# Performance work log

Hardware: AMD Instinct MI355X
Metric: run time of the kernel (lower is better)

The kernel has to match this reference:

```python
import jax, jax.numpy as jnp
import numpy as np

N = 100000      # nodes
E = 1600000     # edges (avg degree 16)
F_IN = 128
HID = 64
OUT = 40
NB = 10000      # batch_nodes
BN_EPS = 1e-5


def setup_inputs() -> dict:
    key = jax.random.key(0)
    ks = jax.random.split(key, 16)
    inp = {}
    inp["features"] = jax.random.normal(ks[0], (N, F_IN), dtype=jnp.float32)
    inp["edge_index"] = jax.random.randint(ks[1], (2, E), 0, N, dtype=jnp.int32)
    inp["batch_nodes"] = jax.random.randint(ks[2], (NB,), 0, N, dtype=jnp.int32)
    # conv1 params (Glorot-ish scale)
    inp["W1"] = jax.random.normal(ks[3], (F_IN, HID), dtype=jnp.float32) * (1.0 / np.sqrt(F_IN))
    inp["b1"] = jnp.zeros((HID,), jnp.float32)
    inp["k2_1"] = jnp.float32(0.5)   # learnable k^2, init 0.5
    # conv2 params
    inp["W2"] = jax.random.normal(ks[4], (HID, OUT), dtype=jnp.float32) * (1.0 / np.sqrt(HID))
    inp["b2"] = jnp.zeros((OUT,), jnp.float32)
    inp["k2_2"] = jnp.float32(0.5)
    # BatchNorm1d(hid) inference params
    inp["g1"] = jax.random.uniform(ks[5], (HID,), jnp.float32, 0.5, 1.5)
    inp["be1"] = jax.random.normal(ks[6], (HID,), jnp.float32) * 0.1
    inp["m1"] = jax.random.normal(ks[7], (HID,), jnp.float32) * 0.1
    inp["v1"] = jax.random.uniform(ks[8], (HID,), jnp.float32, 0.5, 1.5)
    # BatchNorm1d(out) inference params
    inp["g2"] = jax.random.uniform(ks[9], (OUT,), jnp.float32, 0.5, 1.5)
    inp["be2"] = jax.random.normal(ks[10], (OUT,), jnp.float32) * 0.1
    inp["m2"] = jax.random.normal(ks[11], (OUT,), jnp.float32) * 0.1
    inp["v2"] = jax.random.uniform(ks[12], (OUT,), jnp.float32, 0.5, 1.5)
    return inp


def _gcn_propagate(h, src, dst, n):
    # add self loops
    loop = jnp.arange(n, dtype=src.dtype)
    s = jnp.concatenate([src, loop])
    d = jnp.concatenate([dst, loop])
    # symmetric GCN normalization D^-1/2 A_hat D^-1/2
    deg = jnp.zeros((n,), h.dtype).at[d].add(1.0)
    dinv = jax.lax.rsqrt(deg)  # deg >= 1 thanks to self loops
    coef = dinv[s] * dinv[d]   # [E+N]
    msg = coef[:, None] * h[s]                      # gather  [E+N, C]
    agg = jnp.zeros_like(h).at[d].add(msg)          # scatter [N, C]
    return agg


def _helm_conv(x, W, b, k2, src, dst, n):
    h = x @ W                                   # [N, C_out]
    agg = _gcn_propagate(h, src, dst, n)        # A_hat h
    out = agg + k2 * h + b                      # (A_hat + k^2 I) h + b
    # Helmholtz residual: (A_hat - I + k^2 I) h ~ (-L + k^2) h
    resid = agg - h + k2 * h
    helm_loss = jnp.mean(resid * resid)
    return out, helm_loss


def _bn(x, g, be, m, v):
    return (x - m) * jax.lax.rsqrt(v + BN_EPS) * g + be


def reference(features, edge_index, batch_nodes, W1, b1, k2_1, W2, b2, k2_2,
              g1, be1, m1, v1, g2, be2, m2, v2):
    n = features.shape[0]
    src, dst = edge_index[0], edge_index[1]
    x, helm_loss1 = _helm_conv(features, W1, b1, k2_1, src, dst, n)
    x = jnp.tanh(_bn(x, g1, be1, m1, v1))
    # dropout is identity in eval mode
    x, _ = _helm_conv(x, W2, b2, k2_2, src, dst, n)
    x = jnp.tanh(_bn(x, g2, be2, m2, v2))
    logp = jax.nn.log_softmax(x[batch_nodes], axis=1)
    return (logp, helm_loss1)
```

## Files before the change

kernel.cpp:

```cpp
#include <hip/hip_runtime.h>
#include <math.h>


#define BN_EPS 1e-5f
#define NB_BKT 512
#define RCAP 4608
#define PSTRIDE 6656

typedef __attribute__((ext_vector_type(8))) short bf16x8;
typedef __attribute__((ext_vector_type(4))) float f32x4;

__device__ inline unsigned short f2b(float f) {
    unsigned u = __float_as_uint(f);
    unsigned r = (u + 0x7fffu + ((u >> 16) & 1u)) >> 16;
    return (unsigned short)r;
}
__device__ inline float b2f_lo(unsigned u) { return __uint_as_float(u << 16); }
__device__ inline float b2f_hi(unsigned u) { return __uint_as_float(u & 0xffff0000u); }
__device__ inline unsigned pk2(float a, float b) {
    return (unsigned)f2b(a) | ((unsigned)f2b(b) << 16);
}
__device__ inline float tanh_fast(float x) {
    float e = __expf(2.0f * x);
    return 1.0f - 2.0f * __builtin_amdgcn_rcpf(e + 1.0f);
}

__global__ __launch_bounds__(512) void k_init(unsigned* __restrict__ bcnt,
                                              const float* __restrict__ b1,
                                              const float* __restrict__ g1,
                                              const float* __restrict__ be1,
                                              const float* __restrict__ m1,
                                              const float* __restrict__ v1,
                                              const float* __restrict__ b2,
                                              const float* __restrict__ g2,
                                              const float* __restrict__ be2,
                                              const float* __restrict__ m2,
                                              const float* __restrict__ v2,
                                              float* __restrict__ A1,
                                              float* __restrict__ S1,
                                              float* __restrict__ A2,
                                              float* __restrict__ S2) {
    int t = threadIdx.x;
    bcnt[t] = 0;
    if (t < 64) {
        float a = g1[t] * rsqrtf(v1[t] + BN_EPS);
        A1[t] = a;
        S1[t] = (b1[t] - m1[t]) * a + be1[t];
    } else if (t < 104) {
        int c = t - 64;
        float a = g2[c] * rsqrtf(v2[c] + BN_EPS);
        A2[c] = a;
        S2[c] = (b2[c] - m2[c]) * a + be2[c];
    }
}

__global__ __launch_bounds__(256) void k_part(const int* __restrict__ src,
                                              const int* __restrict__ dst, int e,
                                              unsigned* __restrict__ bcnt,
                                              unsigned* __restrict__ part, int nblk) {
    __shared__ unsigned h[NB_BKT];
    __shared__ unsigned gbase[NB_BKT];
    __shared__ unsigned cur[NB_BKT];
    int chunk = ((e + nblk - 1) / nblk + 3) & ~3;
    int c0 = blockIdx.x * chunk;
    int c1 = min(c0 + chunk, e);
    if (c0 >= e) return;
    for (int i = threadIdx.x; i < NB_BKT; i += 256) h[i] = 0;
    __syncthreads();
    for (int i = c0 + threadIdx.x * 4; i < c1; i += 1024) {
        if (i + 3 < c1) {
            int4 d = *(const int4*)&dst[i];
            atomicAdd(&h[(unsigned)d.x >> 8], 1u);
            atomicAdd(&h[(unsigned)d.y >> 8], 1u);
            atomicAdd(&h[(unsigned)d.z >> 8], 1u);
            atomicAdd(&h[(unsigned)d.w >> 8], 1u);
        } else {
            for (int j = i; j < c1; ++j) atomicAdd(&h[(unsigned)dst[j] >> 8], 1u);
        }
    }
    __syncthreads();
    for (int i = threadIdx.x; i < NB_BKT; i += 256) {
        unsigned c = h[i];
        gbase[i] = c ? (i * RCAP + atomicAdd(&bcnt[i], c)) : 0u;
        cur[i] = 0;
    }
    __syncthreads();
    for (int i = c0 + threadIdx.x * 4; i < c1; i += 1024) {
        if (i + 3 < c1) {
            int4 s = *(const int4*)&src[i];
            int4 d = *(const int4*)&dst[i];
            unsigned b0 = (unsigned)d.x >> 8, b1 = (unsigned)d.y >> 8;
            unsigned b2 = (unsigned)d.z >> 8, b3 = (unsigned)d.w >> 8;
            unsigned p0 = gbase[b0] + atomicAdd(&cur[b0], 1u);
            unsigned p1 = gbase[b1] + atomicAdd(&cur[b1], 1u);
            unsigned p2 = gbase[b2] + atomicAdd(&cur[b2], 1u);
            unsigned p3 = gbase[b3] + atomicAdd(&cur[b3], 1u);
            if (p0 < (b0 + 1) * RCAP) part[p0] = (((unsigned)d.x & 255u) << 24) | (unsigned)s.x;
            if (p1 < (b1 + 1) * RCAP) part[p1] = (((unsigned)d.y & 255u) << 24) | (unsigned)s.y;
            if (p2 < (b2 + 1) * RCAP) part[p2] = (((unsigned)d.z & 255u) << 24) | (unsigned)s.z;
            if (p3 < (b3 + 1) * RCAP) part[p3] = (((unsigned)d.w & 255u) << 24) | (unsigned)s.w;
        } else {
            for (int j = i; j < c1; ++j) {
                unsigned b = (unsigned)dst[j] >> 8;
                unsigned p = gbase[b] + atomicAdd(&cur[b], 1u);
                if (p < (b + 1) * RCAP)
                    part[p] = (((unsigned)dst[j] & 255u) << 24) | (unsigned)src[j];
            }
        }
    }
}

__global__ __launch_bounds__(256) void k_deg(const unsigned* __restrict__ part,
                                             const unsigned* __restrict__ bcnt,
                                             unsigned long long* __restrict__ rowinfo,
                                             float* __restrict__ dinv, int n) {
    __shared__ unsigned hist[256];
    __shared__ unsigned sc[256];
    int b = blockIdx.x;
    int cnt = (int)min(bcnt[b], (unsigned)RCAP);
    unsigned base = b * RCAP;
    int dst0 = b << 8;
    int nloc = min(256, n - dst0);
    int t = threadIdx.x;
    hist[t] = 0;
    __syncthreads();
    for (int i = t; i < cnt; i += 256) atomicAdd(&hist[part[base + i] >> 24], 1u);
    __syncthreads();
    unsigned c = hist[t];
    unsigned pcnt = (t < nloc) ? ((c + 7u) & ~7u) : 0u;
    sc[t] = pcnt;
    __syncthreads();
    for (int off = 1; off < 256; off <<= 1) {
        unsigned a = (t >= off) ? sc[t - off] : 0u;
        __syncthreads();
        sc[t] += a;
        __syncthreads();
    }
    if (t < nloc) {
        unsigned beg = (unsigned)b * PSTRIDE + (sc[t] - pcnt);
        rowinfo[dst0 + t] = (unsigned long long)beg | ((unsigned long long)pcnt << 32);
        dinv[dst0 + t] = rsqrtf((float)(c + 1u));
    }
}

__global__ __launch_bounds__(256) void k_scatter(const unsigned* __restrict__ part,
                                                 const unsigned* __restrict__ bcnt,
                                                 const unsigned long long* __restrict__ rowinfo,
                                                 const float* __restrict__ dinv,
                                                 uint2* __restrict__ pairs, int n) {
    __shared__ unsigned cur[256];
    __shared__ unsigned pend[256];
    int b = blockIdx.x;
    int cnt = (int)min(bcnt[b], (unsigned)RCAP);
    unsigned base = b * RCAP;
    int dst0 = b << 8;
    int nloc = min(256, n - dst0);
    int t = threadIdx.x;
    if (t < nloc) {
        unsigned long long ri = rowinfo[dst0 + t];
        cur[t] = (unsigned)ri;
        pend[t] = (unsigned)ri + (unsigned)(ri >> 32);
    } else {
        cur[t] = 0;
        pend[t] = 0;
    }
    __syncthreads();
    for (int i = t; i < cnt; i += 256) {
        unsigned p = part[base + i];
        unsigned loc = p >> 24;
        unsigned s = p & 0xFFFFFFu;
        unsigned pos = atomicAdd(&cur[loc], 1u);
        pairs[pos] = make_uint2(s, __float_as_uint(dinv[s]));
    }
    __syncthreads();
    if (t < nloc) {
        for (unsigned pos = cur[t]; pos < pend[t]; ++pos) pairs[pos] = make_uint2(0u, 0u);
    }
}

__global__ __launch_bounds__(256) void k_gemm1(const float* __restrict__ X,
                                               const float* __restrict__ W,
                                               unsigned* __restrict__ H, int n) {
    __shared__ short wb[4][4][64][8];
    __shared__ float cbuf[4][16][65];
    int t = threadIdx.x;
    for (int s = t; s < 1024; s += 256) {
        int l = s & 63, nt = (s >> 6) & 3, kt = s >> 8;
        int kbase = kt * 32 + ((l >> 4) << 3);
        int nn = nt * 16 + (l & 15);
        bf16x8 v;
#pragma unroll
        for (int j = 0; j < 8; ++j) v[j] = (short)f2b(W[(kbase + j) * 64 + nn]);
        *(bf16x8*)&wb[kt][nt][l][0] = v;
    }
    __syncthreads();
    int lane = t & 63, wave = t >> 6;
    int quad = lane >> 4, m = lane & 15;
    int r0 = blockIdx.x * 64 + wave * 16;
    f32x4 acc[4];
#pragma unroll
    for (int i = 0; i < 4; ++i) acc[i] = (f32x4){0.f, 0.f, 0.f, 0.f};
    int rr = min(r0 + m, n - 1);
    const float* xrow = X + (size_t)rr * 128;
#pragma unroll
    for (int kt = 0; kt < 4; ++kt) {
        int kb = kt * 32 + quad * 8;
        float4 x0 = *(const float4*)&xrow[kb];
        float4 x1 = *(const float4*)&xrow[kb + 4];
        bf16x8 af;
        af[0] = (short)f2b(x0.x); af[1] = (short)f2b(x0.y);
        af[2] = (short)f2b(x0.z); af[3] = (short)f2b(x0.w);
        af[4] = (short)f2b(x1.x); af[5] = (short)f2b(x1.y);
        af[6] = (short)f2b(x1.z); af[7] = (short)f2b(x1.w);
#pragma unroll
        for (int nt = 0; nt < 4; ++nt) {
            bf16x8 bf = *(bf16x8*)&wb[kt][nt][lane][0];
            acc[nt] = __builtin_amdgcn_mfma_f32_16x16x32_bf16(af, bf, acc[nt], 0, 0, 0);
        }
    }
#pragma unroll
    for (int nt = 0; nt < 4; ++nt)
#pragma unroll
        for (int r = 0; r < 4; ++r)
            cbuf[wave][quad * 4 + r][nt * 16 + m] = acc[nt][r];
    __syncthreads();
#pragma unroll
    for (int i = 0; i < 8; ++i) {
        int f = i * 64 + lane;
        int row = f >> 5, cp = f & 31;
        int grow = r0 + row;
        if (grow < n)
            H[(size_t)grow * 32 + cp] =
                pk2(cbuf[wave][row][2 * cp], cbuf[wave][row][2 * cp + 1]);
    }
}

__global__ __launch_bounds__(256) void k_gemm2(const unsigned short* __restrict__ X,
                                               const float* __restrict__ W,
                                               unsigned* __restrict__ H, int n) {
    __shared__ short wb[2][3][64][8];
    __shared__ float cbuf[4][16][49];
    int t = threadIdx.x;
    for (int s = t; s < 384; s += 256) {
        int l = s & 63, nt = (s >> 6) % 3, kt = s / 192;
        int kbase = kt * 32 + ((l >> 4) << 3);
        int c = nt * 16 + (l & 15);
        bf16x8 v;
#pragma unroll
        for (int j = 0; j < 8; ++j)
            v[j] = (c < 40) ? (short)f2b(W[(kbase + j) * 40 + c]) : (short)0;
        *(bf16x8*)&wb[kt][nt][l][0] = v;
    }
    __syncthreads();
    int lane = t & 63, wave = t >> 6;
    int quad = lane >> 4, m = lane & 15;
    int r0 = blockIdx.x * 64 + wave * 16;
    f32x4 acc[3];
#pragma unroll
    for (int i = 0; i < 3; ++i) acc[i] = (f32x4){0.f, 0.f, 0.f, 0.f};
    int rr = min(r0 + m, n - 1);
    const unsigned short* xrow = X + (size_t)rr * 64;
#pragma unroll
    for (int kt = 0; kt < 2; ++kt) {
        bf16x8 af = *(const bf16x8*)&xrow[kt * 32 + quad * 8];
#pragma unroll
        for (int nt = 0; nt < 3; ++nt) {
            bf16x8 bf = *(bf16x8*)&wb[kt][nt][lane][0];
            acc[nt] = __builtin_amdgcn_mfma_f32_16x16x32_bf16(af, bf, acc[nt], 0, 0, 0);
        }
    }
#pragma unroll
    for (int nt = 0; nt < 3; ++nt)
#pragma unroll
        for (int r = 0; r < 4; ++r)
            cbuf[wave][quad * 4 + r][nt * 16 + m] = acc[nt][r];
    __syncthreads();
#pragma unroll
    for (int i = 0; i < 5; ++i) {
        int f = i * 64 + lane;
        int row = f / 20, cp = f % 20;
        int grow = r0 + row;
        if (grow < n)
            H[(size_t)grow * 20 + cp] =
                pk2(cbuf[wave][row][2 * cp], cbuf[wave][row][2 * cp + 1]);
    }
}

__global__ __launch_bounds__(256) void k_conv1(const unsigned long long* __restrict__ rowinfo,
                                               const uint2* __restrict__ pairs,
                                               const float* __restrict__ dinv,
                                               const unsigned* __restrict__ h1,
                                               unsigned* __restrict__ x,
                                               const float* __restrict__ A1,
                                               const float* __restrict__ S1,
                                               const float* __restrict__ k2p,
                                               float* __restrict__ partial, int n) {
    int lane = threadIdx.x & 63, wave = threadIdx.x >> 6;
    int half = lane >> 5, c2 = lane & 31;
    int node = blockIdx.x * 4 + wave;
    float r2 = 0.0f;
    if (node < n) {
        unsigned long long ri = rowinfo[node];
        unsigned beg = (unsigned)ri, pdeg = (unsigned)(ri >> 32);
        float dd = dinv[node];
        unsigned hp = h1[(unsigned)node * 32u + (unsigned)c2];
        float hx = b2f_lo(hp), hy = b2f_hi(hp);
        float ax = half ? 0.f : dd * hx;
        float ay = half ? 0.f : dd * hy;
        for (unsigned eb = 0; eb < pdeg; eb += 8) {
            unsigned bi = beg + eb + (unsigned)half * 4u;
            uint4 q0 = *(const uint4*)&pairs[bi];
            uint4 q1 = *(const uint4*)&pairs[bi + 2];
            unsigned p0 = h1[(q0.x << 5) + (unsigned)c2];
            unsigned p1 = h1[(q0.z << 5) + (unsigned)c2];
            unsigned p2 = h1[(q1.x << 5) + (unsigned)c2];
            unsigned p3 = h1[(q1.z << 5) + (unsigned)c2];
            float c0 = __uint_as_float(q0.y), c1 = __uint_as_float(q0.w);
            float c2f = __uint_as_float(q1.y), c3 = __uint_as_float(q1.w);
            ax += c0 * b2f_lo(p0); ay += c0 * b2f_hi(p0);
            ax += c1 * b2f_lo(p1); ay += c1 * b2f_hi(p1);
            ax += c2f * b2f_lo(p2); ay += c2f * b2f_hi(p2);
            ax += c3 * b2f_lo(p3); ay += c3 * b2f_hi(p3);
        }
        ax += __shfl_xor(ax, 32, 64);
        ay += __shfl_xor(ay, 32, 64);
        if (half == 0) {
            float a_x = dd * ax, a_y = dd * ay;
            float k2 = k2p[0];
            float rx = a_x + (k2 - 1.0f) * hx;
            float ry = a_y + (k2 - 1.0f) * hy;
            r2 = rx * rx + ry * ry;
            float2 Ap = *(const float2*)&A1[2 * c2];
            float2 Sp = *(const float2*)&S1[2 * c2];
            float xnx = tanh_fast((a_x + k2 * hx) * Ap.x + Sp.x);
            float xny = tanh_fast((a_y + k2 * hy) * Ap.y + Sp.y);
            x[(unsigned)node * 32u + (unsigned)c2] = pk2(xnx, xny);
        }
    }
    for (int off = 32; off; off >>= 1) r2 += __shfl_xor(r2, off, 64);
    __shared__ float red[4];
    if (lane == 0) red[wave] = r2;
    __syncthreads();
    if (threadIdx.x == 0) partial[blockIdx.x] = red[0] + red[1] + red[2] + red[3];
}

__global__ __launch_bounds__(1024) void k_loss(const float* __restrict__ partial,
                                               int nparts, float* __restrict__ out,
                                               size_t idx, float inv_cnt) {
    float s = 0.f;
    for (int i = threadIdx.x; i < nparts; i += 1024) s += partial[i];
    for (int off = 32; off; off >>= 1) s += __shfl_xor(s, off, 64);
    __shared__ float red[16];
    int wv = threadIdx.x >> 6, ln = threadIdx.x & 63;
    if (ln == 0) red[wv] = s;
    __syncthreads();
    if (threadIdx.x == 0) {
        float t = 0.f;
        for (int i = 0; i < 16; ++i) t += red[i];
        out[idx] = t * inv_cnt;
    }
}

__global__ __launch_bounds__(256) void k_conv2(const int* __restrict__ bn,
                                               const unsigned long long* __restrict__ rowinfo,
                                               const uint2* __restrict__ pairs,
                                               const float* __restrict__ dinv,
                                               const unsigned* __restrict__ h2,
                                               const float* __restrict__ A2,
                                               const float* __restrict__ S2,
                                               const float* __restrict__ k2p,
                                               float* __restrict__ out, int nb) {
    int lane = threadIdx.x & 63, wave = threadIdx.x >> 6;
    int wid = blockIdx.x * 4 + wave;
    if (wid >= nb) return;
    int half = lane >> 5, c2 = lane & 31;
    unsigned p = (unsigned)min(c2, 19);
    int node = bn[wid];
    unsigned long long ri = rowinfo[node];
    unsigned beg = (unsigned)ri, pdeg = (unsigned)(ri >> 32);
    float dd = dinv[node];
    unsigned hp = h2[(unsigned)node * 20u + p];
    float hx = b2f_lo(hp), hy = b2f_hi(hp);
    float ax = half ? 0.f : dd * hx;
    float ay = half ? 0.f : dd * hy;
    for (unsigned eb = 0; eb < pdeg; eb += 8) {
        unsigned bi = beg + eb + (unsigned)half * 4u;
        uint4 q0 = *(const uint4*)&pairs[bi];
        uint4 q1 = *(const uint4*)&pairs[bi + 2];
        unsigned p0 = h2[q0.x * 20u + p];
        unsigned p1 = h2[q0.z * 20u + p];
        unsigned p2 = h2[q1.x * 20u + p];
        unsigned p3 = h2[q1.z * 20u + p];
        float c0 = __uint_as_float(q0.y), c1 = __uint_as_float(q0.w);
        float c2f = __uint_as_float(q1.y), c3 = __uint_as_float(q1.w);
        ax += c0 * b2f_lo(p0); ay += c0 * b2f_hi(p0);
        ax += c1 * b2f_lo(p1); ay += c1 * b2f_hi(p1);
        ax += c2f * b2f_lo(p2); ay += c2f * b2f_hi(p2);
        ax += c3 * b2f_lo(p3); ay += c3 * b2f_hi(p3);
    }
    ax += __shfl_xor(ax, 32, 64);
    ay += __shfl_xor(ay, 32, 64);
    float k2 = k2p[0];
    float2 Ap = *(const float2*)&A2[2 * p];
    float2 Sp = *(const float2*)&S2[2 * p];
    float tx = tanh_fast((dd * ax + k2 * hx) * Ap.x + Sp.x);
    float ty = tanh_fast((dd * ay + k2 * hy) * Ap.y + Sp.y);
    bool act = (half == 0) && (c2 < 20);
    float mx = act ? fmaxf(tx, ty) : -INFINITY;
    for (int off = 32; off; off >>= 1) mx = fmaxf(mx, __shfl_xor(mx, off, 64));
    float es = act ? (__expf(tx - mx) + __expf(ty - mx)) : 0.f;
    for (int off = 32; off; off >>= 1) es += __shfl_xor(es, off, 64);
    if (act) {
        float ls = mx + __logf(es);
        float2 o = make_float2(tx - ls, ty - ls);
        *(float2*)&out[(size_t)wid * 40 + 2 * p] = o;
    }
}

extern "C" void kernel_launch(void* const* d_in, const int* in_sizes, int n_in,
                              void* d_out, int out_size, void* d_ws, size_t ws_size,
                              hipStream_t stream) {
    const float* features = (const float*)d_in[0];
    const int* edge_index = (const int*)d_in[1];
    const int* batch_nodes = (const int*)d_in[2];
    const float* W1 = (const float*)d_in[3];
    const float* b1 = (const float*)d_in[4];
    const float* k2_1 = (const float*)d_in[5];
    const float* W2 = (const float*)d_in[6];
    const float* b2 = (const float*)d_in[7];
    const float* k2_2 = (const float*)d_in[8];
    const float* g1 = (const float*)d_in[9];
    const float* be1 = (const float*)d_in[10];
    const float* m1 = (const float*)d_in[11];
    const float* v1 = (const float*)d_in[12];
    const float* g2 = (const float*)d_in[13];
    const float* be2 = (const float*)d_in[14];
    const float* m2 = (const float*)d_in[15];
    const float* v2 = (const float*)d_in[16];

    const int N = in_sizes[0] / 128;
    const int E = in_sizes[1] / 2;
    const int NB = in_sizes[2];
    const int* src = edge_index;
    const int* dst = edge_index + E;
    const int NPART = (N + 3) / 4;
    const int NBKT = (N + 255) >> 8;
    const int PBLK = 256;

    unsigned* ws = (unsigned*)d_ws;
    auto align64 = [](size_t o) { return (o + 63) & ~(size_t)63; };
    size_t o = 0;
    unsigned long long* rowinfo = (unsigned long long*)(ws + o); o = align64(o + 2 * (size_t)N);
    float* dinv = (float*)(ws + o);       o = align64(o + N);
    float* A1 = (float*)(ws + o);         o = align64(o + 64);
    float* S1 = (float*)(ws + o);         o = align64(o + 64);
    float* A2 = (float*)(ws + o);         o = align64(o + 64);
    float* S2 = (float*)(ws + o);         o = align64(o + 64);
    unsigned* bcnt = ws + o;              o = align64(o + NB_BKT);
    float* partial = (float*)(ws + o);    o = align64(o + NPART);
    uint2* pairs = (uint2*)(ws + o);      o = align64(o + 2 * (size_t)NB_BKT * PSTRIDE);
    unsigned* h1 = ws + o;                o = align64(o + (size_t)N * 32);
    unsigned* x = ws + o;                 o = align64(o + (size_t)N * 32);
    unsigned* h2 = ws + o;                o = align64(o + (size_t)N * 20);
    unsigned* part = h1;

    k_init<<<1, 512, 0, stream>>>(bcnt, b1, g1, be1, m1, v1, b2, g2, be2, m2, v2,
                                  A1, S1, A2, S2);
    k_part<<<PBLK, 256, 0, stream>>>(src, dst, E, bcnt, part, PBLK);
    k_deg<<<NBKT, 256, 0, stream>>>(part, bcnt, rowinfo, dinv, N);
    k_scatter<<<NBKT, 256, 0, stream>>>(part, bcnt, rowinfo, dinv, pairs, N);

    k_gemm1<<<(N + 63) / 64, 256, 0, stream>>>(features, W1, h1, N);
    k_conv1<<<NPART, 256, 0, stream>>>(rowinfo, pairs, dinv, h1, x, A1, S1, k2_1,
                                       partial, N);
    k_loss<<<1, 1024, 0, stream>>>(partial, NPART, (float*)d_out, (size_t)NB * 40,
                                   1.0f / ((float)N * 64.0f));
    k_gemm2<<<(N + 63) / 64, 256, 0, stream>>>((const unsigned short*)x, W2, h2, N);
    k_conv2<<<(NB + 3) / 4, 256, 0, stream>>>(batch_nodes, rowinfo, pairs, dinv, h2,
                                              A2, S2, k2_2, (float*)d_out, NB);
}
```

Before: 247.9 us.

## Pack edge coefficient into source index word and fold small kernels together

Edge pairs shrink from 8 bytes (index plus fp32 coefficient) to one 32-bit word holding a 17-bit source index and a truncated bf16-like dinv. This roughly halves CSR traffic in both conv kernels, which now process 16 edges per iteration with rows padded to 16. The init kernel is replaced by a memset plus BN-constant setup inside k_deg, the loss reduction moves into an extra block of k_conv2, and the partition kernel uses more blocks. The risks are coefficient precision loss and a node index limit of 2^17.

```diff
diff --git a/kernel.cpp b/kernel.cpp
--- a/kernel.cpp
+++ b/kernel.cpp
@@ -5,7 +5,7 @@
 #define BN_EPS 1e-5f
 #define NB_BKT 512
 #define RCAP 4608
-#define PSTRIDE 6656
+#define PSTRIDE 8448
 
 typedef __attribute__((ext_vector_type(8))) short bf16x8;
 typedef __attribute__((ext_vector_type(4))) float f32x4;
@@ -24,34 +24,8 @@
     float e = __expf(2.0f * x);
     return 1.0f - 2.0f * __builtin_amdgcn_rcpf(e + 1.0f);
 }
-
-__global__ __launch_bounds__(512) void k_init(unsigned* __restrict__ bcnt,
-                                              const float* __restrict__ b1,
-                                              const float* __restrict__ g1,
-                                              const float* __restrict__ be1,
-                                              const float* __restrict__ m1,
-                                              const float* __restrict__ v1,
-                                              const float* __restrict__ b2,
-                                              const float* __restrict__ g2,
-                                              const float* __restrict__ be2,
-                                              const float* __restrict__ m2,
-                                              const float* __restrict__ v2,
-                                              float* __restrict__ A1,
-                                              float* __restrict__ S1,
-                                              float* __restrict__ A2,
-                                              float* __restrict__ S2) {
-    int t = threadIdx.x;
-    bcnt[t] = 0;
-    if (t < 64) {
-        float a = g1[t] * rsqrtf(v1[t] + BN_EPS);
-        A1[t] = a;
-        S1[t] = (b1[t] - m1[t]) * a + be1[t];
-    } else if (t < 104) {
-        int c = t - 64;
-        float a = g2[c] * rsqrtf(v2[c] + BN_EPS);
-        A2[c] = a;
-        S2[c] = (b2[c] - m2[c]) * a + be2[c];
-    }
+__device__ inline float qcoef(unsigned q) {
+    return __uint_as_float((q >> 1) & 0xFFFF0000u);
 }
 
 __global__ __launch_bounds__(256) void k_part(const int* __restrict__ src,
@@ -113,7 +87,21 @@
 __global__ __launch_bounds__(256) void k_deg(const unsigned* __restrict__ part,
                                              const unsigned* __restrict__ bcnt,
                                              unsigned long long* __restrict__ rowinfo,
-                                             float* __restrict__ dinv, int n) {
+                                             float* __restrict__ dinv, int n,
+                                             const float* __restrict__ b1,
+                                             const float* __restrict__ g1,
+                                             const float* __restrict__ be1,
+                                             const float* __restrict__ m1,
+                                             const float* __restrict__ v1,
+                                             const float* __restrict__ b2p,
+                                             const float* __restrict__ g2,
+                                             const float* __restrict__ be2,
+                                             const float* __restrict__ m2,
+                                             const float* __restrict__ v2,
+                                             float* __restrict__ A1,
+                                             float* __restrict__ S1,
+                                             float* __restrict__ A2,
+                                             float* __restrict__ S2) {
     __shared__ unsigned hist[256];
     __shared__ unsigned sc[256];
     int b = blockIdx.x;
@@ -127,7 +115,7 @@
     for (int i = t; i < cnt; i += 256) atomicAdd(&hist[part[base + i] >> 24], 1u);
     __syncthreads();
     unsigned c = hist[t];
-    unsigned pcnt = (t < nloc) ? ((c + 7u) & ~7u) : 0u;
+    unsigned pcnt = (t < nloc) ? ((c + 15u) & ~15u) : 0u;
     sc[t] = pcnt;
     __syncthreads();
     for (int off = 1; off < 256; off <<= 1) {
@@ -141,13 +129,25 @@
         rowinfo[dst0 + t] = (unsigned long long)beg | ((unsigned long long)pcnt << 32);
         dinv[dst0 + t] = rsqrtf((float)(c + 1u));
     }
+    if (b == 0) {
+        if (t < 64) {
+            float a = g1[t] * rsqrtf(v1[t] + BN_EPS);
+            A1[t] = a;
+            S1[t] = (b1[t] - m1[t]) * a + be1[t];
+        } else if (t < 104) {
+            int cc = t - 64;
+            float a = g2[cc] * rsqrtf(v2[cc] + BN_EPS);
+            A2[cc] = a;
+            S2[cc] = (b2p[cc] - m2[cc]) * a + be2[cc];
+        }
+    }
 }
 
 __global__ __launch_bounds__(256) void k_scatter(const unsigned* __restrict__ part,
                                                  const unsigned* __restrict__ bcnt,
                                                  const unsigned long long* __restrict__ rowinfo,
                                                  const float* __restrict__ dinv,
-                                                 uint2* __restrict__ pairs, int n) {
+                                                 unsigned* __restrict__ qs, int n) {
     __shared__ unsigned cur[256];
     __shared__ unsigned pend[256];
     int b = blockIdx.x;
@@ -169,12 +169,14 @@
         unsigned p = part[base + i];
         unsigned loc = p >> 24;
         unsigned s = p & 0xFFFFFFu;
+        unsigned du = __float_as_uint(dinv[s]);
+        unsigned q = (((du + 0x8000u) & 0xFFFF0000u) << 1) | s;
         unsigned pos = atomicAdd(&cur[loc], 1u);
-        pairs[pos] = make_uint2(s, __float_as_uint(dinv[s]));
+        qs[pos] = q;
     }
     __syncthreads();
     if (t < nloc) {
-        for (unsigned pos = cur[t]; pos < pend[t]; ++pos) pairs[pos] = make_uint2(0u, 0u);
+        for (unsigned pos = cur[t]; pos < pend[t]; ++pos) qs[pos] = 0u;
     }
 }
 
@@ -287,7 +289,7 @@
 }
 
 __global__ __launch_bounds__(256) void k_conv1(const unsigned long long* __restrict__ rowinfo,
-                                               const uint2* __restrict__ pairs,
+                                               const unsigned* __restrict__ qs,
                                                const float* __restrict__ dinv,
                                                const unsigned* __restrict__ h1,
                                                unsigned* __restrict__ x,
@@ -297,7 +299,7 @@
                                                float* __restrict__ partial, int n) {
     int lane = threadIdx.x & 63, wave = threadIdx.x >> 6;
     int half = lane >> 5, c2 = lane & 31;
-    int node = blockIdx.x * 4 + wave;
+    int node = __builtin_amdgcn_readfirstlane(blockIdx.x * 4 + wave);
     float r2 = 0.0f;
     if (node < n) {
         unsigned long long ri = rowinfo[node];
@@ -307,20 +309,28 @@
         float hx = b2f_lo(hp), hy = b2f_hi(hp);
         float ax = half ? 0.f : dd * hx;
         float ay = half ? 0.f : dd * hy;
-        for (unsigned eb = 0; eb < pdeg; eb += 8) {
-            unsigned bi = beg + eb + (unsigned)half * 4u;
-            uint4 q0 = *(const uint4*)&pairs[bi];
-            uint4 q1 = *(const uint4*)&pairs[bi + 2];
-            unsigned p0 = h1[(q0.x << 5) + (unsigned)c2];
-            unsigned p1 = h1[(q0.z << 5) + (unsigned)c2];
-            unsigned p2 = h1[(q1.x << 5) + (unsigned)c2];
-            unsigned p3 = h1[(q1.z << 5) + (unsigned)c2];
-            float c0 = __uint_as_float(q0.y), c1 = __uint_as_float(q0.w);
-            float c2f = __uint_as_float(q1.y), c3 = __uint_as_float(q1.w);
+        for (unsigned eb = 0; eb < pdeg; eb += 16) {
+            unsigned bi = beg + eb + (unsigned)half * 8u;
+            uint4 q0 = *(const uint4*)&qs[bi];
+            uint4 q1 = *(const uint4*)&qs[bi + 4];
+            unsigned p0 = h1[((q0.x & 0x1FFFFu) << 5) + (unsigned)c2];
+            unsigned p1 = h1[((q0.y & 0x1FFFFu) << 5) + (unsigned)c2];
+            unsigned p2 = h1[((q0.z & 0x1FFFFu) << 5) + (unsigned)c2];
+            unsigned p3 = h1[((q0.w & 0x1FFFFu) << 5) + (unsigned)c2];
+            unsigned p4 = h1[((q1.x & 0x1FFFFu) << 5) + (unsigned)c2];
+            unsigned p5 = h1[((q1.y & 0x1FFFFu) << 5) + (unsigned)c2];
+            unsigned p6 = h1[((q1.z & 0x1FFFFu) << 5) + (unsigned)c2];
+            unsigned p7 = h1[((q1.w & 0x1FFFFu) << 5) + (unsigned)c2];
+            float c0 = qcoef(q0.x), c1 = qcoef(q0.y), c2f = qcoef(q0.z), c3 = qcoef(q0.w);
+            float c4 = qcoef(q1.x), c5 = qcoef(q1.y), c6 = qcoef(q1.z), c7 = qcoef(q1.w);
             ax += c0 * b2f_lo(p0); ay += c0 * b2f_hi(p0);
             ax += c1 * b2f_lo(p1); ay += c1 * b2f_hi(p1);
             ax += c2f * b2f_lo(p2); ay += c2f * b2f_hi(p2);
             ax += c3 * b2f_lo(p3); ay += c3 * b2f_hi(p3);
+            ax += c4 * b2f_lo(p4); ay += c4 * b2f_hi(p4);
+            ax += c5 * b2f_lo(p5); ay += c5 * b2f_hi(p5);
+            ax += c6 * b2f_lo(p6); ay += c6 * b2f_hi(p6);
+            ax += c7 * b2f_lo(p7); ay += c7 * b2f_hi(p7);
         }
         ax += __shfl_xor(ax, 32, 64);
         ay += __shfl_xor(ay, 32, 64);
@@ -344,33 +354,29 @@
     if (threadIdx.x == 0) partial[blockIdx.x] = red[0] + red[1] + red[2] + red[3];
 }
 
-__global__ __launch_bounds__(1024) void k_loss(const float* __restrict__ partial,
-                                               int nparts, float* __restrict__ out,
-                                               size_t idx, float inv_cnt) {
-    float s = 0.f;
-    for (int i = threadIdx.x; i < nparts; i += 1024) s += partial[i];
-    for (int off = 32; off; off >>= 1) s += __shfl_xor(s, off, 64);
-    __shared__ float red[16];
-    int wv = threadIdx.x >> 6, ln = threadIdx.x & 63;
-    if (ln == 0) red[wv] = s;
-    __syncthreads();
-    if (threadIdx.x == 0) {
-        float t = 0.f;
-        for (int i = 0; i < 16; ++i) t += red[i];
-        out[idx] = t * inv_cnt;
-    }
-}
-
 __global__ __launch_bounds__(256) void k_conv2(const int* __restrict__ bn,
                                                const unsigned long long* __restrict__ rowinfo,
-                                               const uint2* __restrict__ pairs,
+                                               const unsigned* __restrict__ qs,
                                                const float* __restrict__ dinv,
                                                const unsigned* __restrict__ h2,
                                                const float* __restrict__ A2,
                                                const float* __restrict__ S2,
                                                const float* __restrict__ k2p,
+                                               const float* __restrict__ partial,
+                                               int nparts, float inv_cnt,
                                                float* __restrict__ out, int nb) {
     int lane = threadIdx.x & 63, wave = threadIdx.x >> 6;
+    if (blockIdx.x == gridDim.x - 1) {
+        float s = 0.f;
+        for (int i = threadIdx.x; i < nparts; i += 256) s += partial[i];
+        for (int off = 32; off; off >>= 1) s += __shfl_xor(s, off, 64);
+        __shared__ float red[4];
+        if (lane == 0) red[wave] = s;
+        __syncthreads();
+        if (threadIdx.x == 0)
+            out[(size_t)nb * 40] = (red[0] + red[1] + red[2] + red[3]) * inv_cnt;
+        return;
+    }
     int wid = blockIdx.x * 4 + wave;
     if (wid >= nb) return;
     int half = lane >> 5, c2 = lane & 31;
@@ -383,20 +389,28 @@
     float hx = b2f_lo(hp), hy = b2f_hi(hp);
     float ax = half ? 0.f : dd * hx;
     float ay = half ? 0.f : dd * hy;
-    for (unsigned eb = 0; eb < pdeg; eb += 8) {
-        unsigned bi = beg + eb + (unsigned)half * 4u;
-        uint4 q0 = *(const uint4*)&pairs[bi];
-        uint4 q1 = *(const uint4*)&pairs[bi + 2];
-        unsigned p0 = h2[q0.x * 20u + p];
-        unsigned p1 = h2[q0.z * 20u + p];
-        unsigned p2 = h2[q1.x * 20u + p];
-        unsigned p3 = h2[q1.z * 20u + p];
-        float c0 = __uint_as_float(q0.y), c1 = __uint_as_float(q0.w);
-        float c2f = __uint_as_float(q1.y), c3 = __uint_as_float(q1.w);
+    for (unsigned eb = 0; eb < pdeg; eb += 16) {
+        unsigned bi = beg + eb + (unsigned)half * 8u;
+        uint4 q0 = *(const uint4*)&qs[bi];
+        uint4 q1 = *(const uint4*)&qs[bi + 4];
+        unsigned p0 = h2[(q0.x & 0x1FFFFu) * 20u + p];
+        unsigned p1 = h2[(q0.y & 0x1FFFFu) * 20u + p];
+        unsigned p2 = h2[(q0.z & 0x1FFFFu) * 20u + p];
+        unsigned p3 = h2[(q0.w & 0x1FFFFu) * 20u + p];
+        unsigned p4 = h2[(q1.x & 0x1FFFFu) * 20u + p];
+        unsigned p5 = h2[(q1.y & 0x1FFFFu) * 20u + p];
+        unsigned p6 = h2[(q1.z & 0x1FFFFu) * 20u + p];
+        unsigned p7 = h2[(q1.w & 0x1FFFFu) * 20u + p];
+        float c0 = qcoef(q0.x), c1 = qcoef(q0.y), c2f = qcoef(q0.z), c3 = qcoef(q0.w);
+        float c4 = qcoef(q1.x), c5 = qcoef(q1.y), c6 = qcoef(q1.z), c7 = qcoef(q1.w);
         ax += c0 * b2f_lo(p0); ay += c0 * b2f_hi(p0);
         ax += c1 * b2f_lo(p1); ay += c1 * b2f_hi(p1);
         ax += c2f * b2f_lo(p2); ay += c2f * b2f_hi(p2);
         ax += c3 * b2f_lo(p3); ay += c3 * b2f_hi(p3);
+        ax += c4 * b2f_lo(p4); ay += c4 * b2f_hi(p4);
+        ax += c5 * b2f_lo(p5); ay += c5 * b2f_hi(p5);
+        ax += c6 * b2f_lo(p6); ay += c6 * b2f_hi(p6);
+        ax += c7 * b2f_lo(p7); ay += c7 * b2f_hi(p7);
     }
     ax += __shfl_xor(ax, 32, 64);
     ay += __shfl_xor(ay, 32, 64);
@@ -445,7 +459,7 @@
     const int* dst = edge_index + E;
     const int NPART = (N + 3) / 4;
     const int NBKT = (N + 255) >> 8;
-    const int PBLK = 256;
+    const int PBLK = 512;
 
     unsigned* ws = (unsigned*)d_ws;
     auto align64 = [](size_t o) { return (o + 63) & ~(size_t)63; };
@@ -458,24 +472,24 @@
     float* S2 = (float*)(ws + o);         o = align64(o + 64);
     unsigned* bcnt = ws + o;              o = align64(o + NB_BKT);
     float* partial = (float*)(ws + o);    o = align64(o + NPART);
-    uint2* pairs = (uint2*)(ws + o);      o = align64(o + 2 * (size_t)NB_BKT * PSTRIDE);
+    unsigned* qs = ws + o;                o = align64(o + (size_t)NB_BKT * PSTRIDE);
     unsigned* h1 = ws + o;                o = align64(o + (size_t)N * 32);
     unsigned* x = ws + o;                 o = align64(o + (size_t)N * 32);
     unsigned* h2 = ws + o;                o = align64(o + (size_t)N * 20);
     unsigned* part = h1;
 
-    k_init<<<1, 512, 0, stream>>>(bcnt, b1, g1, be1, m1, v1, b2, g2, be2, m2, v2,
-                                  A1, S1, A2, S2);
+    hipMemsetAsync(bcnt, 0, NB_BKT * sizeof(unsigned), stream);
     k_part<<<PBLK, 256, 0, stream>>>(src, dst, E, bcnt, part, PBLK);
-    k_deg<<<NBKT, 256, 0, stream>>>(part, bcnt, rowinfo, dinv, N);
-    k_scatter<<<NBKT, 256, 0, stream>>>(part, bcnt, rowinfo, dinv, pairs, N);
+    k_deg<<<NBKT, 256, 0, stream>>>(part, bcnt, rowinfo, dinv, N, b1, g1, be1, m1,
+                                    v1, b2, g2, be2, m2, v2, A1, S1, A2, S2);
+    k_scatter<<<NBKT, 256, 0, stream>>>(part, bcnt, rowinfo, dinv, qs, N);
 
     k_gemm1<<<(N + 63) / 64, 256, 0, stream>>>(features, W1, h1, N);
-    k_conv1<<<NPART, 256, 0, stream>>>(rowinfo, pairs, dinv, h1, x, A1, S1, k2_1,
+    k_conv1<<<NPART, 256, 0, stream>>>(rowinfo, qs, dinv, h1, x, A1, S1, k2_1,
                                        partial, N);
-    k_loss<<<1, 1024, 0, stream>>>(partial, NPART, (float*)d_out, (size_t)NB * 40,
-                                   1.0f / ((float)N * 64.0f));
     k_gemm2<<<(N + 63) / 64, 256, 0, stream>>>((const unsigned short*)x, W2, h2, N);
-    k_conv2<<<(NB + 3) / 4, 256, 0, stream>>>(batch_nodes, rowinfo, pairs, dinv, h2,
-                                              A2, S2, k2_2, (float*)d_out, NB);
-}
+    k_conv2<<<(NB + 3) / 4 + 1, 256, 0, stream>>>(batch_nodes, rowinfo, qs, dinv, h2,
+                                                  A2, S2, k2_2, partial, NPART,
+                                                  1.0f / ((float)N * 64.0f),
+                                                  (float*)d_out, NB);
+}
```

Result: slower. 259.6 us (+4.7%).
